# Optimization experiments

Hardware: AMD Instinct MI355X
Metric: run time of the kernel (lower is better)

## Reference

```python
import jax, jax.numpy as jnp
import numpy as np

CONV_ORDER = 3


def _aggr_norm(L, x):
    # neighborhood_size = row sums of operator; 1/ns with non-finite -> 0
    inv = 1.0 / jnp.sum(L, axis=1)
    inv = jnp.where(jnp.isfinite(inv), inv, 0.0)
    x = inv[:, None] * x
    return jnp.where(jnp.isfinite(x), x, 0.0)


def _chebyshev_conv(L, x, conv_order=CONV_ORDER, aggr_norm=True):
    # Returns [N, C, conv_order]: X[...,k] = norm(L @ X[...,k-1]), X[...,-1 base] = x
    def step(carry, _):
        y = L @ carry
        if aggr_norm:
            y = _aggr_norm(L, y)
        return y, y
    _, X = jax.lax.scan(step, x, None, length=conv_order)  # [K, N, C]
    return jnp.moveaxis(X, 0, -1)  # [N, C, K]


def setup_inputs() -> dict:
    key = jax.random.key(0)
    ks = jax.random.split(key, 13)
    N0, N1, N2, C = 4096, 8192, 4096, 16
    w_scale = 1.414 * np.sqrt(2.0 / (C + C))  # xavier_normal-like
    return {
        "x_0": jax.random.normal(ks[0], (N0, C), jnp.float32),
        "x_1": jax.random.normal(ks[1], (N1, C), jnp.float32),
        "x_2": jax.random.normal(ks[2], (N2, C), jnp.float32),
        "laplacian_0": jax.random.normal(ks[3], (N0, N0), jnp.float32),
        "laplacian_down_1": jax.random.normal(ks[4], (N1, N1), jnp.float32),
        "laplacian_up_1": jax.random.normal(ks[5], (N1, N1), jnp.float32),
        "laplacian_down_2": jax.random.normal(ks[6], (N2, N2), jnp.float32),
        "laplacian_up_2": jax.random.normal(ks[7], (N2, N2), jnp.float32),
        "b1": jax.random.normal(ks[8], (N0, N1), jnp.float32),
        "b2": jax.random.normal(ks[9], (N1, N2), jnp.float32),
        "weight_0": w_scale * jax.random.normal(ks[10], (C, C, 2 + 2 * CONV_ORDER), jnp.float32),
        "weight_1": w_scale * jax.random.normal(ks[11], (C, C, 6 * CONV_ORDER + 3), jnp.float32),
        "weight_2": w_scale * jax.random.normal(ks[12], (C, C, 4 * CONV_ORDER + 2), jnp.float32),
    }


def reference(x_0, x_1, x_2, laplacian_0, laplacian_down_1, laplacian_up_1,
              laplacian_down_2, laplacian_up_2, b1, b2,
              weight_0, weight_1, weight_2):
    # Node-space convolution (the torch forward returns only y_0; the edge/face
    # branches are dead code w.r.t. the returned value and are omitted).
    x_0_lap = _chebyshev_conv(laplacian_0, x_0)                 # [N0, C, K]
    x_0_to_0 = jnp.concatenate([x_0[:, :, None], x_0_lap], axis=2)
    x_1_to_0_upper = b1 @ x_1                                   # [N0, C]
    x_1_to_0_lap = _chebyshev_conv(laplacian_0, x_1_to_0_upper)
    x_1_to_0 = jnp.concatenate([x_1_to_0_upper[:, :, None], x_1_to_0_lap], axis=2)
    x_0_all = jnp.concatenate([x_0_to_0, x_1_to_0], axis=2)     # [N0, C, 2+2K]
    y_0 = jnp.einsum('nik,iok->no', x_0_all, weight_0)
    return y_0
```

## Files before the change

kernel.cpp:

```cpp
#include <hip/hip_runtime.h>
#include <hip/hip_bf16.h>
#include <math.h>

#define N0 4096
#define NM1 8192

#define OFF_U   0
#define OFF_XL1 65536
#define OFF_XL2 131072
#define OFF_UL1 196608
#define OFF_UL2 262144
#define OFF_INV 327680
#define OFF_PB  331776
#define OFF_PX  593920
#define OFF_PU  1118208
#define OFF_PRS 1642496

template<int NV>
__device__ __forceinline__ void red_scatter(float* v, const int d, const int lane) {
  const bool up = (lane & d) != 0;
  #pragma unroll
  for (int i = 0; i < NV; ++i) {
    float send = up ? v[i] : v[i + NV];
    float recv = __shfl_xor(send, d);
    float keep = up ? v[i + NV] : v[i];
    v[i] = keep + recv;
  }
}

__global__ __launch_bounds__(256)
void b1_kernel(const float* __restrict__ A,
               const float* __restrict__ X,
               float* __restrict__ pP)
{
  __shared__ float4 Bs[1024];
  const int tid  = threadIdx.x;
  const int wv   = tid >> 6;
  const int lane = tid & 63;
  const int q    = lane >> 5;
  const int ml   = lane & 31;
  const int s    = blockIdx.x & 3;
  const int rg   = blockIdx.x >> 2;
  const int row0 = rg * 8 + wv * 2;
  const int mb   = s * 2048;

  const float* A0 = A + (size_t)row0 * NM1 + mb + ml * 4;
  const float* A1 = A0 + NM1;
  const int j0 = q * 2;
  const int jj = tid & 3;
  const int mt = tid >> 2;

  float acc[16];
  #pragma unroll
  for (int i = 0; i < 16; ++i) acc[i] = 0.0f;

  #pragma unroll 1
  for (int ch = 0; ch < 8; ++ch) {
    __syncthreads();
    #pragma unroll
    for (int k = 0; k < 4; ++k) {
      const int m = mt + 64 * k;
      Bs[(m * 4 + jj) ^ ((m >> 2) & 7)] =
          *(const float4*)(X + (size_t)(mb + ch * 256 + m) * 16 + jj * 4);
    }
    __syncthreads();
    #pragma unroll
    for (int il = 0; il < 2; ++il) {
      const int it = ch * 2 + il;
      const float4 a0 = *(const float4*)(A0 + it * 128);
      const float4 a1 = *(const float4*)(A1 + it * 128);
      #pragma unroll
      for (int v = 0; v < 4; ++v) {
        const int mm = il * 128 + ml * 4 + v;
        const int h = (mm >> 2) & 7;
        const float4 b0  = Bs[(mm * 4 + j0) ^ h];
        const float4 b1v = Bs[(mm * 4 + j0 + 1) ^ h];
        const float av0 = (&a0.x)[v];
        const float av1 = (&a1.x)[v];
        acc[0]  += av0 * b0.x;   acc[1]  += av0 * b0.y;
        acc[2]  += av0 * b0.z;   acc[3]  += av0 * b0.w;
        acc[4]  += av0 * b1v.x;  acc[5]  += av0 * b1v.y;
        acc[6]  += av0 * b1v.z;  acc[7]  += av0 * b1v.w;
        acc[8]  += av1 * b0.x;   acc[9]  += av1 * b0.y;
        acc[10] += av1 * b0.z;   acc[11] += av1 * b0.w;
        acc[12] += av1 * b1v.x;  acc[13] += av1 * b1v.y;
        acc[14] += av1 * b1v.z;  acc[15] += av1 * b1v.w;
      }
    }
  }

  red_scatter<8>(acc, 1, lane);
  red_scatter<4>(acc, 2, lane);
  red_scatter<2>(acc, 4, lane);
  red_scatter<1>(acc, 8, lane);
  const float tot = acc[0] + __shfl_xor(acc[0], 16);

  if (ml < 16) {
    const int r = ml & 1;
    const int c = 4 * ((ml >> 1) & 1) + 2 * ((ml >> 2) & 1) + ((ml >> 3) & 1);
    pP[(size_t)(s * 65536) + (row0 + r) * 16 + q * 8 + c] = tot;
  }
}

__global__ void finalize_u_kernel(const float* __restrict__ pP,
                                  float* __restrict__ u) {
  const int idx = blockIdx.x * 256 + threadIdx.x;
  u[idx] = pP[idx] + pP[65536 + idx] + pP[131072 + idx] + pP[196608 + idx];
}

template<bool RS>
__global__ __launch_bounds__(256)
void cheb_kernel(const float* __restrict__ A,
                 const float* __restrict__ cx,
                 const float* __restrict__ cu,
                 float* __restrict__ pX,
                 float* __restrict__ pU,
                 float* __restrict__ pRS)
{
  __shared__ float4 Bs[1024];
  const int tid  = threadIdx.x;
  const int wv   = tid >> 6;
  const int lane = tid & 63;
  const int q    = lane >> 3;
  const int ml   = lane & 7;
  const int s    = blockIdx.x & 7;
  const int rg   = blockIdx.x >> 3;
  const int row0 = rg * 16 + wv * 4;
  const int mb   = s * 512;

  const float* Ab = A + (size_t)row0 * N0 + mb + ml * 4;
  const int jj = tid & 7;
  const int mt = tid >> 3;
  const float* sbase = (jj < 4) ? cx : cu;
  const int joff = (jj & 3) * 4;

  float acc[16];
  #pragma unroll
  for (int i = 0; i < 16; ++i) acc[i] = 0.0f;
  float rs[4] = {0.0f, 0.0f, 0.0f, 0.0f};

  #pragma unroll 1
  for (int ch = 0; ch < 4; ++ch) {
    __syncthreads();
    #pragma unroll
    for (int k = 0; k < 4; ++k) {
      const int m = mt + 32 * k;
      Bs[(m * 8 + jj) ^ ((m >> 2) & 7)] =
          *(const float4*)(sbase + (size_t)(mb + ch * 128 + m) * 16 + joff);
    }
    __syncthreads();
    #pragma unroll
    for (int il = 0; il < 4; ++il) {
      const int it = ch * 4 + il;
      float4 b[4];
      #pragma unroll
      for (int v = 0; v < 4; ++v) {
        const int mm = il * 32 + ml * 4 + v;
        b[v] = Bs[(mm * 8 + q) ^ ((mm >> 2) & 7)];
      }
      #pragma unroll
      for (int r = 0; r < 4; ++r) {
        const float4 a = *(const float4*)(Ab + (size_t)r * N0 + it * 32);
        #pragma unroll
        for (int v = 0; v < 4; ++v) {
          const float av = (&a.x)[v];
          acc[r*4+0] += av * b[v].x;  acc[r*4+1] += av * b[v].y;
          acc[r*4+2] += av * b[v].z;  acc[r*4+3] += av * b[v].w;
          if constexpr (RS) rs[r] += av;
        }
      }
    }
  }

  red_scatter<8>(acc, 1, lane);
  red_scatter<4>(acc, 2, lane);
  red_scatter<2>(acc, 4, lane);
  const int r   = 2 * (ml & 1) + ((ml >> 1) & 1);
  const int ch2 = (ml >> 2) & 1;
  float* base = (q >> 2) ? pU : pX;
  *(float2*)(base + (size_t)(s * 65536) + (row0 + r) * 16 + (q & 3) * 4 + ch2 * 2) =
      make_float2(acc[0], acc[1]);

  if constexpr (RS) {
    red_scatter<2>(rs, 1, lane);
    red_scatter<1>(rs, 2, lane);
    const float rsum = rs[0] + __shfl_xor(rs[0], 4);
    if (q == 0 && ml < 4) {
      const int rr = 2 * (ml & 1) + ((ml >> 1) & 1);
      pRS[s * N0 + row0 + rr] = rsum;
    }
  }
}

__global__ void norm1_kernel(const float* __restrict__ pX,
                             const float* __restrict__ pU,
                             const float* __restrict__ pRS,
                             float* __restrict__ inv,
                             float* __restrict__ ox,
                             float* __restrict__ ou) {
  const int idx = blockIdx.x * 256 + threadIdx.x;
  const int row = idx >> 4;
  float rsv = 0.0f;
  #pragma unroll
  for (int s2 = 0; s2 < 8; ++s2) rsv += pRS[s2 * N0 + row];
  float iv = 1.0f / rsv;
  if (!isfinite(iv)) iv = 0.0f;
  if ((idx & 15) == 0) inv[row] = iv;
  float xv = 0.0f, uv = 0.0f;
  #pragma unroll
  for (int s2 = 0; s2 < 8; ++s2) { xv += pX[s2*65536 + idx]; uv += pU[s2*65536 + idx]; }
  xv *= iv; uv *= iv;
  ox[idx] = isfinite(xv) ? xv : 0.0f;
  ou[idx] = isfinite(uv) ? uv : 0.0f;
}

__global__ void norm23_kernel(const float* __restrict__ pX,
                              const float* __restrict__ pU,
                              const float* __restrict__ inv,
                              float* __restrict__ ox,
                              float* __restrict__ ou) {
  const int idx = blockIdx.x * 256 + threadIdx.x;
  const float iv = inv[idx >> 4];
  float xv = 0.0f, uv = 0.0f;
  #pragma unroll
  for (int s2 = 0; s2 < 8; ++s2) { xv += pX[s2*65536 + idx]; uv += pU[s2*65536 + idx]; }
  xv *= iv; uv *= iv;
  ox[idx] = isfinite(xv) ? xv : 0.0f;
  ou[idx] = isfinite(uv) ? uv : 0.0f;
}

__global__ void einsum_kernel(const float* __restrict__ x0,
                              const float* __restrict__ xl1,
                              const float* __restrict__ xl2,
                              const float* __restrict__ u,
                              const float* __restrict__ ul1,
                              const float* __restrict__ ul2,
                              const float* __restrict__ pX,
                              const float* __restrict__ pU,
                              const float* __restrict__ inv,
                              const float* __restrict__ W,
                              float* __restrict__ y) {
  __shared__ float Wl[2048];
  __shared__ float xs[16 * 128];
  const int t = threadIdx.x;
  const int row0 = blockIdx.x * 16;
  #pragma unroll
  for (int k = 0; k < 8; ++k) Wl[t + 256 * k] = W[t + 256 * k];
  const int r = t >> 4;
  const int i = t & 15;
  const int g = (row0 + r) * 16 + i;
  const float iv = inv[row0 + r];
  float x3 = 0.0f, u3 = 0.0f;
  #pragma unroll
  for (int s2 = 0; s2 < 8; ++s2) { x3 += pX[s2*65536 + g]; u3 += pU[s2*65536 + g]; }
  x3 *= iv; u3 *= iv;
  if (!isfinite(x3)) x3 = 0.0f;
  if (!isfinite(u3)) u3 = 0.0f;
  xs[r*128 + 0*16 + i] = x0[g];
  xs[r*128 + 1*16 + i] = xl1[g];
  xs[r*128 + 2*16 + i] = xl2[g];
  xs[r*128 + 3*16 + i] = x3;
  xs[r*128 + 4*16 + i] = u[g];
  xs[r*128 + 5*16 + i] = ul1[g];
  xs[r*128 + 6*16 + i] = ul2[g];
  xs[r*128 + 7*16 + i] = u3;
  __syncthreads();
  const int o = t & 15;
  float a = 0.0f;
  #pragma unroll
  for (int ii = 0; ii < 16; ++ii) {
    #pragma unroll
    for (int k = 0; k < 8; ++k)
      a += xs[r*128 + k*16 + ii] * Wl[(ii*16 + o)*8 + k];
  }
  y[(row0 + r) * 16 + o] = a;
}

extern "C" void kernel_launch(void* const* d_in, const int* in_sizes, int n_in,
                              void* d_out, int out_size, void* d_ws, size_t ws_size,
                              hipStream_t stream) {
  (void)in_sizes; (void)n_in; (void)out_size; (void)ws_size;
  const float* x0 = (const float*)d_in[0];
  const float* x1 = (const float*)d_in[1];
  const float* L0 = (const float*)d_in[3];
  const float* B1 = (const float*)d_in[8];
  const float* W0 = (const float*)d_in[10];

  float* ws  = (float*)d_ws;
  float* u   = ws + OFF_U;
  float* xl1 = ws + OFF_XL1;
  float* xl2 = ws + OFF_XL2;
  float* ul1 = ws + OFF_UL1;
  float* ul2 = ws + OFF_UL2;
  float* inv = ws + OFF_INV;
  float* pB  = ws + OFF_PB;
  float* pX  = ws + OFF_PX;
  float* pU  = ws + OFF_PU;
  float* pRS = ws + OFF_PRS;

  b1_kernel<<<2048, 256, 0, stream>>>(B1, x1, pB);
  finalize_u_kernel<<<256, 256, 0, stream>>>(pB, u);

  cheb_kernel<true><<<2048, 256, 0, stream>>>(L0, x0, u, pX, pU, pRS);
  norm1_kernel<<<256, 256, 0, stream>>>(pX, pU, pRS, inv, xl1, ul1);
  cheb_kernel<false><<<2048, 256, 0, stream>>>(L0, xl1, ul1, pX, pU, pRS);
  norm23_kernel<<<256, 256, 0, stream>>>(pX, pU, inv, xl2, ul2);
  cheb_kernel<false><<<2048, 256, 0, stream>>>(L0, xl2, ul2, pX, pU, pRS);

  einsum_kernel<<<256, 256, 0, stream>>>(x0, xl1, xl2, u, ul1, ul2,
                                         pX, pU, inv, W0, (float*)d_out);
}
```

Baseline: 139.7 us.

## Fuse all stages into a persistent mega-kernel with hierarchical grid barriers

Replaces the eight separate launches (b1 GEMV, finalize, three Chebyshev passes, two norms, einsum) with one persistent kernel. Blocks loop over tiles, and the stages are separated by a two-level atomic grid barrier. The finalize kernel is removed by summing the four b1 partials directly inside the first Chebyshev load and inside the einsum. This is meant to cut launch gaps and tail effects between the small, dependent stages. The cost is barrier spin overhead and a reliance on every block being co-resident, with the grid size taken from the occupancy query.

```diff
diff --git a/kernel.cpp b/kernel.cpp
--- a/kernel.cpp
+++ b/kernel.cpp
@@ -5,16 +5,37 @@
 #define N0 4096
 #define NM1 8192
 
-#define OFF_U   0
-#define OFF_XL1 65536
-#define OFF_XL2 131072
-#define OFF_UL1 196608
-#define OFF_UL2 262144
-#define OFF_INV 327680
-#define OFF_PB  331776
-#define OFF_PX  593920
-#define OFF_PU  1118208
-#define OFF_PRS 1642496
+#define OFF_XL1 0
+#define OFF_XL2 65536
+#define OFF_UL1 131072
+#define OFF_UL2 196608
+#define OFF_INV 262144
+#define OFF_PB  266240
+#define OFF_PX  528384
+#define OFF_PU  1052672
+#define OFF_PRS 1576960
+#define OFF_BAR 1609728
+#define REL_OFF 6240
+#define BAR_INTS 6256
+
+__device__ __forceinline__ void grid_barrier(int* bar, int bi, int ngroups) {
+  __syncthreads();
+  if (threadIdx.x == 0) {
+    const int gid = blockIdx.x >> 5;
+    int* grp  = bar + (bi * 65 + gid) * 16;
+    int* root = bar + (bi * 65 + 64) * 16;
+    int* rel  = bar + REL_OFF;
+    if (__hip_atomic_fetch_add(grp, 1, __ATOMIC_ACQ_REL, __HIP_MEMORY_SCOPE_AGENT) == 31) {
+      if (__hip_atomic_fetch_add(root, 1, __ATOMIC_ACQ_REL, __HIP_MEMORY_SCOPE_AGENT) == ngroups - 1) {
+        __hip_atomic_store(rel, bi + 1, __ATOMIC_RELEASE, __HIP_MEMORY_SCOPE_AGENT);
+      }
+    }
+    while (__hip_atomic_load(rel, __ATOMIC_ACQUIRE, __HIP_MEMORY_SCOPE_AGENT) < bi + 1) {
+      __builtin_amdgcn_s_sleep(2);
+    }
+  }
+  __syncthreads();
+}
 
 template<int NV>
 __device__ __forceinline__ void red_scatter(float* v, const int d, const int lane) {
@@ -28,19 +49,17 @@
   }
 }
 
-__global__ __launch_bounds__(256)
-void b1_kernel(const float* __restrict__ A,
-               const float* __restrict__ X,
-               float* __restrict__ pP)
-{
-  __shared__ float4 Bs[1024];
+__device__ __forceinline__ void b1_phase(const float* __restrict__ A,
+                                         const float* __restrict__ X,
+                                         float* __restrict__ pP,
+                                         float4* Bs, int bid) {
   const int tid  = threadIdx.x;
   const int wv   = tid >> 6;
   const int lane = tid & 63;
   const int q    = lane >> 5;
   const int ml   = lane & 31;
-  const int s    = blockIdx.x & 3;
-  const int rg   = blockIdx.x >> 2;
+  const int s    = bid & 3;
+  const int rg   = bid >> 2;
   const int row0 = rg * 8 + wv * 2;
   const int mb   = s * 2048;
 
@@ -102,29 +121,21 @@
   }
 }
 
-__global__ void finalize_u_kernel(const float* __restrict__ pP,
-                                  float* __restrict__ u) {
-  const int idx = blockIdx.x * 256 + threadIdx.x;
-  u[idx] = pP[idx] + pP[65536 + idx] + pP[131072 + idx] + pP[196608 + idx];
-}
-
-template<bool RS>
-__global__ __launch_bounds__(256)
-void cheb_kernel(const float* __restrict__ A,
-                 const float* __restrict__ cx,
-                 const float* __restrict__ cu,
-                 float* __restrict__ pX,
-                 float* __restrict__ pU,
-                 float* __restrict__ pRS)
-{
-  __shared__ float4 Bs[1024];
+template<bool RS, bool SUMU>
+__device__ __forceinline__ void cheb_phase(const float* __restrict__ A,
+                                           const float* __restrict__ cx,
+                                           const float* __restrict__ cu,
+                                           float* __restrict__ pX,
+                                           float* __restrict__ pU,
+                                           float* __restrict__ pRS,
+                                           float4* Bs, int bid) {
   const int tid  = threadIdx.x;
   const int wv   = tid >> 6;
   const int lane = tid & 63;
   const int q    = lane >> 3;
   const int ml   = lane & 7;
-  const int s    = blockIdx.x & 7;
-  const int rg   = blockIdx.x >> 3;
+  const int s    = bid & 7;
+  const int rg   = bid >> 3;
   const int row0 = rg * 16 + wv * 4;
   const int mb   = s * 512;
 
@@ -145,8 +156,25 @@
     #pragma unroll
     for (int k = 0; k < 4; ++k) {
       const int m = mt + 32 * k;
-      Bs[(m * 8 + jj) ^ ((m >> 2) & 7)] =
-          *(const float4*)(sbase + (size_t)(mb + ch * 128 + m) * 16 + joff);
+      float4 val;
+      if constexpr (SUMU) {
+        if (jj >= 4) {
+          const float* pb = cu + (size_t)(mb + ch * 128 + m) * 16 + joff;
+          const float4 t0 = *(const float4*)(pb);
+          const float4 t1 = *(const float4*)(pb + 65536);
+          const float4 t2 = *(const float4*)(pb + 131072);
+          const float4 t3 = *(const float4*)(pb + 196608);
+          val = make_float4(t0.x + t1.x + t2.x + t3.x,
+                            t0.y + t1.y + t2.y + t3.y,
+                            t0.z + t1.z + t2.z + t3.z,
+                            t0.w + t1.w + t2.w + t3.w);
+        } else {
+          val = *(const float4*)(cx + (size_t)(mb + ch * 128 + m) * 16 + joff);
+        }
+      } else {
+        val = *(const float4*)(sbase + (size_t)(mb + ch * 128 + m) * 16 + joff);
+      }
+      Bs[(m * 8 + jj) ^ ((m >> 2) & 7)] = val;
     }
     __syncthreads();
     #pragma unroll
@@ -192,20 +220,26 @@
   }
 }
 
-__global__ void norm1_kernel(const float* __restrict__ pX,
-                             const float* __restrict__ pU,
-                             const float* __restrict__ pRS,
-                             float* __restrict__ inv,
-                             float* __restrict__ ox,
-                             float* __restrict__ ou) {
+template<bool FIRST>
+__device__ __forceinline__ void norm_phase(const float* __restrict__ pX,
+                                           const float* __restrict__ pU,
+                                           const float* __restrict__ pRS,
+                                           float* __restrict__ inv,
+                                           float* __restrict__ ox,
+                                           float* __restrict__ ou) {
   const int idx = blockIdx.x * 256 + threadIdx.x;
   const int row = idx >> 4;
-  float rsv = 0.0f;
-  #pragma unroll
-  for (int s2 = 0; s2 < 8; ++s2) rsv += pRS[s2 * N0 + row];
-  float iv = 1.0f / rsv;
-  if (!isfinite(iv)) iv = 0.0f;
-  if ((idx & 15) == 0) inv[row] = iv;
+  float iv;
+  if constexpr (FIRST) {
+    float rsv = 0.0f;
+    #pragma unroll
+    for (int s2 = 0; s2 < 8; ++s2) rsv += pRS[s2 * N0 + row];
+    iv = 1.0f / rsv;
+    if (!isfinite(iv)) iv = 0.0f;
+    if ((idx & 15) == 0) inv[row] = iv;
+  } else {
+    iv = inv[row];
+  }
   float xv = 0.0f, uv = 0.0f;
   #pragma unroll
   for (int s2 = 0; s2 < 8; ++s2) { xv += pX[s2*65536 + idx]; uv += pU[s2*65536 + idx]; }
@@ -214,34 +248,20 @@
   ou[idx] = isfinite(uv) ? uv : 0.0f;
 }
 
-__global__ void norm23_kernel(const float* __restrict__ pX,
-                              const float* __restrict__ pU,
-                              const float* __restrict__ inv,
-                              float* __restrict__ ox,
-                              float* __restrict__ ou) {
-  const int idx = blockIdx.x * 256 + threadIdx.x;
-  const float iv = inv[idx >> 4];
-  float xv = 0.0f, uv = 0.0f;
-  #pragma unroll
-  for (int s2 = 0; s2 < 8; ++s2) { xv += pX[s2*65536 + idx]; uv += pU[s2*65536 + idx]; }
-  xv *= iv; uv *= iv;
-  ox[idx] = isfinite(xv) ? xv : 0.0f;
-  ou[idx] = isfinite(uv) ? uv : 0.0f;
-}
-
-__global__ void einsum_kernel(const float* __restrict__ x0,
-                              const float* __restrict__ xl1,
-                              const float* __restrict__ xl2,
-                              const float* __restrict__ u,
-                              const float* __restrict__ ul1,
-                              const float* __restrict__ ul2,
-                              const float* __restrict__ pX,
-                              const float* __restrict__ pU,
-                              const float* __restrict__ inv,
-                              const float* __restrict__ W,
-                              float* __restrict__ y) {
-  __shared__ float Wl[2048];
-  __shared__ float xs[16 * 128];
+__device__ __forceinline__ void einsum_phase(const float* __restrict__ x0,
+                                             const float* __restrict__ xl1,
+                                             const float* __restrict__ xl2,
+                                             const float* __restrict__ pB,
+                                             const float* __restrict__ ul1,
+                                             const float* __restrict__ ul2,
+                                             const float* __restrict__ pX,
+                                             const float* __restrict__ pU,
+                                             const float* __restrict__ inv,
+                                             const float* __restrict__ W,
+                                             float* __restrict__ y,
+                                             float* smem) {
+  float* Wl = smem;
+  float* xs = smem + 2048;
   const int t = threadIdx.x;
   const int row0 = blockIdx.x * 16;
   #pragma unroll
@@ -256,11 +276,12 @@
   x3 *= iv; u3 *= iv;
   if (!isfinite(x3)) x3 = 0.0f;
   if (!isfinite(u3)) u3 = 0.0f;
+  const float uval = pB[g] + pB[65536 + g] + pB[131072 + g] + pB[196608 + g];
   xs[r*128 + 0*16 + i] = x0[g];
   xs[r*128 + 1*16 + i] = xl1[g];
   xs[r*128 + 2*16 + i] = xl2[g];
   xs[r*128 + 3*16 + i] = x3;
-  xs[r*128 + 4*16 + i] = u[g];
+  xs[r*128 + 4*16 + i] = uval;
   xs[r*128 + 5*16 + i] = ul1[g];
   xs[r*128 + 6*16 + i] = ul2[g];
   xs[r*128 + 7*16 + i] = u3;
@@ -274,6 +295,57 @@
       a += xs[r*128 + k*16 + ii] * Wl[(ii*16 + o)*8 + k];
   }
   y[(row0 + r) * 16 + o] = a;
+}
+
+__global__ void init_bar_kernel(int* bar) {
+  for (int i = threadIdx.x; i < BAR_INTS; i += 256) bar[i] = 0;
+}
+
+__global__ __launch_bounds__(256)
+void mega_kernel(const float* __restrict__ x0, const float* __restrict__ x1,
+                 const float* __restrict__ L0, const float* __restrict__ B1,
+                 const float* __restrict__ W0, float* __restrict__ ws,
+                 int* __restrict__ bar, float* __restrict__ y) {
+  __shared__ float4 Bs[1024];
+  float* xl1 = ws + OFF_XL1;
+  float* xl2 = ws + OFF_XL2;
+  float* ul1 = ws + OFF_UL1;
+  float* ul2 = ws + OFF_UL2;
+  float* inv = ws + OFF_INV;
+  float* pB  = ws + OFF_PB;
+  float* pX  = ws + OFF_PX;
+  float* pU  = ws + OFF_PU;
+  float* pRS = ws + OFF_PRS;
+  const int G = gridDim.x;
+  const int ngroups = G >> 5;
+
+  #pragma unroll 1
+  for (int t = blockIdx.x; t < 2048; t += G) b1_phase(B1, x1, pB, Bs, t);
+  grid_barrier(bar, 0, ngroups);
+
+  #pragma unroll 1
+  for (int t = blockIdx.x; t < 2048; t += G)
+    cheb_phase<true, true>(L0, x0, pB, pX, pU, pRS, Bs, t);
+  grid_barrier(bar, 1, ngroups);
+
+  if (blockIdx.x < 256) norm_phase<true>(pX, pU, pRS, inv, xl1, ul1);
+  grid_barrier(bar, 2, ngroups);
+
+  #pragma unroll 1
+  for (int t = blockIdx.x; t < 2048; t += G)
+    cheb_phase<false, false>(L0, xl1, ul1, pX, pU, pRS, Bs, t);
+  grid_barrier(bar, 3, ngroups);
+
+  if (blockIdx.x < 256) norm_phase<false>(pX, pU, pRS, inv, xl2, ul2);
+  grid_barrier(bar, 4, ngroups);
+
+  #pragma unroll 1
+  for (int t = blockIdx.x; t < 2048; t += G)
+    cheb_phase<false, false>(L0, xl2, ul2, pX, pU, pRS, Bs, t);
+  grid_barrier(bar, 5, ngroups);
+
+  if (blockIdx.x < 256)
+    einsum_phase(x0, xl1, xl2, pB, ul1, ul2, pX, pU, inv, W0, y, (float*)Bs);
 }
 
 extern "C" void kernel_launch(void* const* d_in, const int* in_sizes, int n_in,
@@ -286,27 +358,16 @@
   const float* B1 = (const float*)d_in[8];
   const float* W0 = (const float*)d_in[10];
 
-  float* ws  = (float*)d_ws;
-  float* u   = ws + OFF_U;
-  float* xl1 = ws + OFF_XL1;
-  float* xl2 = ws + OFF_XL2;
-  float* ul1 = ws + OFF_UL1;
-  float* ul2 = ws + OFF_UL2;
-  float* inv = ws + OFF_INV;
-  float* pB  = ws + OFF_PB;
-  float* pX  = ws + OFF_PX;
-  float* pU  = ws + OFF_PU;
-  float* pRS = ws + OFF_PRS;
-
-  b1_kernel<<<2048, 256, 0, stream>>>(B1, x1, pB);
-  finalize_u_kernel<<<256, 256, 0, stream>>>(pB, u);
-
-  cheb_kernel<true><<<2048, 256, 0, stream>>>(L0, x0, u, pX, pU, pRS);
-  norm1_kernel<<<256, 256, 0, stream>>>(pX, pU, pRS, inv, xl1, ul1);
-  cheb_kernel<false><<<2048, 256, 0, stream>>>(L0, xl1, ul1, pX, pU, pRS);
-  norm23_kernel<<<256, 256, 0, stream>>>(pX, pU, inv, xl2, ul2);
-  cheb_kernel<false><<<2048, 256, 0, stream>>>(L0, xl2, ul2, pX, pU, pRS);
-
-  einsum_kernel<<<256, 256, 0, stream>>>(x0, xl1, xl2, u, ul1, ul2,
-                                         pX, pU, inv, W0, (float*)d_out);
-}
+  float* ws = (float*)d_ws;
+  int* bar = (int*)(ws + OFF_BAR);
+
+  int occ = 0;
+  hipOccupancyMaxActiveBlocksPerMultiprocessor(&occ, mega_kernel, 256, 0);
+  if (occ < 1) occ = 1;
+  if (occ > 8) occ = 8;
+  int G = occ * 256;
+  if (G > 2048) G = 2048;
+
+  init_bar_kernel<<<1, 256, 0, stream>>>(bar);
+  mega_kernel<<<G, 256, 0, stream>>>(x0, x1, L0, B1, W0, ws, bar, (float*)d_out);
+}
```

After: 394.8 us. 2.83x slower.
